# Kernel tuning notes

Measured on AMD Instinct MI355X. Metric: run time of the kernel, lower is better.

## Reference

```python
import math
import jax, jax.numpy as jnp
import numpy as np

B, C, T = 8, 512, 1024
H = 8
HD = C // H  # 64
CLIP = 4
COUT = 512


def setup_inputs() -> dict:
    key = jax.random.key(0)
    ks = jax.random.split(key, 12)
    s_qkv = math.sqrt(6.0 / (C + C))  # xavier_uniform for 1x1 conv
    queries = jax.random.normal(ks[0], (B, C, T), dtype=jnp.float32)
    Wq = jax.random.uniform(ks[1], (C, C), jnp.float32, -s_qkv, s_qkv)
    bq = jnp.zeros((C,), jnp.float32)
    Wk = jax.random.uniform(ks[2], (C, C), jnp.float32, -s_qkv, s_qkv)
    bk = jnp.zeros((C,), jnp.float32)
    Wv = jax.random.uniform(ks[3], (C, C), jnp.float32, -s_qkv, s_qkv)
    bv = jnp.zeros((C,), jnp.float32)
    Wp = jax.random.normal(ks[4], (COUT, C), jnp.float32) * (1.0 / math.sqrt(C))
    bp = jnp.zeros((COUT,), jnp.float32)
    w_std = HD ** (-0.5)
    wK = jax.random.normal(ks[5], (1, 2 * CLIP + 1, HD), jnp.float32) * w_std
    wV = jax.random.normal(ks[6], (1, 2 * CLIP + 1, HD), jnp.float32) * w_std
    return {"queries": queries, "Wq": Wq, "bq": bq, "Wk": Wk, "bk": bk,
            "Wv": Wv, "bv": bv, "Wp": Wp, "bp": bp, "wK": wK, "wV": wV}


def _get_relative_embedding(w, length):
    # w: [1, 2*CLIP+1, HD] -> [1, 2*length-1, HD]
    emb_len = 2 * length - 1
    p = max(emb_len - 2 * CLIP - 1, 0)
    pc, pf = (p + 1) // 2, p // 2  # ceil, floor of p/2
    w = jnp.pad(w, ((0, 0), (pc, pf), (0, 0)))
    idx = max(CLIP + 1 - length, 0)
    return w[:, idx:idx + emb_len]


def _rel_to_abs(x):
    # x: [B, H, L, 2L-1] -> [B, H, L, L]  (pad/shift trick)
    b, h, L, _ = x.shape
    x = jnp.pad(x, ((0, 0), (0, 0), (0, 0), (0, 1)))           # [b,h,L,2L]
    x = x.reshape(b, h, L * 2 * L)
    x = jnp.pad(x, ((0, 0), (0, 0), (0, L - 1)))
    x = x.reshape(b, h, L + 1, 2 * L - 1)
    return x[:, :, :L, L - 1:]


def _abs_to_rel(x):
    # x: [B, H, L, L] -> [B, H, L, 2L-1]
    b, h, L, _ = x.shape
    x = jnp.pad(x, ((0, 0), (0, 0), (0, 0), (0, L - 1)))       # [b,h,L,2L-1]
    x = x.reshape(b, h, L * (2 * L - 1))
    x = jnp.pad(x, ((0, 0), (0, 0), (L, 0)))
    x = x.reshape(b, h, L, 2 * L)
    return x[:, :, :, 1:]


def reference(queries, Wq, bq, Wk, bk, Wv, bv, Wp, bp, wK, wV):
    b, c, t = queries.shape
    scale = 1.0 / math.sqrt(HD)
    # 1x1-conv projections (self-attention: keys = values = queries)
    q = jnp.einsum('oc,bct->bot', Wq, queries) + bq[None, :, None]
    k = jnp.einsum('oc,bct->bot', Wk, queries) + bk[None, :, None]
    v = jnp.einsum('oc,bct->bot', Wv, queries) + bv[None, :, None]
    # [b, H, t, HD]
    q = q.reshape(b, H, HD, t).transpose(0, 1, 3, 2)
    k = k.reshape(b, H, HD, t).transpose(0, 1, 3, 2)
    v = v.reshape(b, H, HD, t).transpose(0, 1, 3, 2)
    scores = jnp.einsum('bhtd,bhsd->bhts', q, k) * scale
    # relative-position key bias
    rel_k = _get_relative_embedding(wK, t)[0]                  # [2t-1, HD]
    pos = jnp.einsum('bhtd,md->bhtm', q, rel_k)                # [b,H,t,2t-1]
    scores = scores + _rel_to_abs(pos) * scale
    alignments = jax.nn.softmax(scores, axis=-1)
    attn = jnp.einsum('bhts,bhsd->bhtd', alignments, v)
    # relative-position value bias
    rel_v = _get_relative_embedding(wV, t)[0]                  # [2t-1, HD]
    pos_rel = _abs_to_rel(alignments)                          # [b,H,t,2t-1]
    attn = attn + jnp.einsum('bhtm,md->bhtd', pos_rel, rel_v)
    attn = attn.transpose(0, 1, 3, 2).reshape(b, c, t)         # [b, C, t]
    out = jnp.einsum('oc,bct->bot', Wp, attn) + bp[None, :, None]
    return out, alignments
```

## Files before the change

### kernel.cpp

```cpp
#include <hip/hip_runtime.h>
#include <hip/hip_bf16.h>

#define BB 8
#define CC 512
#define TT 1024
#define HH 8
#define HD 64
#define CLIPW 4
#define NCOUT 512

using bf16 = __hip_bfloat16;
typedef __bf16 bf16x8_t __attribute__((ext_vector_type(8)));
typedef __bf16 bf16x4_t __attribute__((ext_vector_type(4)));
typedef float f32x4_t __attribute__((ext_vector_type(4)));

__global__ __launch_bounds__(256) void prep_w(
    const float* __restrict__ Wq, const float* __restrict__ Wk,
    const float* __restrict__ Wv, const float* __restrict__ Wp,
    bf16* __restrict__ wqf, bf16* __restrict__ wkf,
    bf16* __restrict__ wvf, bf16* __restrict__ wpf) {
  const int which = blockIdx.y;
  const float* W = (which == 0) ? Wq : (which == 1) ? Wk : (which == 2) ? Wv : Wp;
  bf16* F = (which == 0) ? wqf : (which == 1) ? wkf : (which == 2) ? wvf : wpf;
  const int gid = blockIdx.x * 256 + threadIdx.x;
  const int l = gid & 63;
  const int fid = gid >> 6;
  const int ct = fid & 15, ot = fid >> 4;
  const int sl = l & 15, g = l >> 4;
  const float* src = W + (size_t)(ot * 16 + sl) * CC + ct * 32 + g * 8;
  bf16x8_t p;
#pragma unroll
  for (int j = 0; j < 8; ++j) p[j] = (__bf16)src[j];
  *(bf16x8_t*)(F + (size_t)fid * 512 + l * 8) = p;
}

__global__ __launch_bounds__(256) void prep_x(
    const float* __restrict__ X, bf16* __restrict__ xfrag) {
  __shared__ float Xs[32][72];
  const int b = blockIdx.z, ct = blockIdx.y, tq = blockIdx.x;
  const int c0 = ct * 32, t0 = tq * 64;
  const int tid = threadIdx.x;
  {
    const int ci = tid >> 4;
    const int t4 = (tid & 15) * 4;
#pragma unroll
    for (int cp = 0; cp < 2; ++cp) {
      const int c = cp * 16 + ci;
      const float4 x4 = *(const float4*)&X[((size_t)b * CC + c0 + c) * TT + t0 + t4];
      *(float4*)&Xs[c][t4] = x4;
    }
  }
  __syncthreads();
  const int l = tid & 63, fr = tid >> 6;
  const int sl = l & 15, g = l >> 4;
  bf16x8_t p;
#pragma unroll
  for (int j = 0; j < 8; ++j) p[j] = (__bf16)Xs[g * 8 + j][fr * 16 + sl];
  *(bf16x8_t*)(xfrag + (((size_t)b * 64 + tq * 4 + fr) * 16 + ct) * 512 + l * 8) = p;
}

__global__ __launch_bounds__(256) void gemm_qkv2(
    const bf16* __restrict__ xfrag,
    const bf16* __restrict__ wqf, const bf16* __restrict__ wkf,
    const bf16* __restrict__ wvf,
    const float* __restrict__ bq, const float* __restrict__ bk,
    const float* __restrict__ bv,
    bf16* __restrict__ qfrag, bf16* __restrict__ kfrag, bf16* __restrict__ vfrag) {
  __shared__ __align__(16) float Cs[64 * 68];
  const int y  = blockIdx.y;
  const int m  = y >> 3;
  const int o0 = (y & 7) * 64;
  const int t0 = blockIdx.x * 64;
  const int b  = blockIdx.z;
  const bf16* WF = (m == 0) ? wqf : (m == 1) ? wkf : wvf;
  const float* bias = (m == 0) ? bq : (m == 1) ? bk : bv;

  const int tid = threadIdx.x;
  const int w = tid >> 6, l = tid & 63, g = l >> 4, sl = l & 15;
  const int wr = w >> 1, wc = w & 1;
  const int ot0 = (o0 >> 4) + wr * 2;
  const int tt0 = (t0 >> 4) + wc * 2;

  f32x4_t acc[2][2] = {};
#pragma unroll 4
  for (int ct = 0; ct < 16; ++ct) {
    bf16x8_t a[2], bb[2];
#pragma unroll
    for (int mm = 0; mm < 2; ++mm)
      a[mm] = *(const bf16x8_t*)(WF + ((size_t)(ot0 + mm) * 16 + ct) * 512 + l * 8);
#pragma unroll
    for (int nn = 0; nn < 2; ++nn)
      bb[nn] = *(const bf16x8_t*)(xfrag + (((size_t)b * 64 + tt0 + nn) * 16 + ct) * 512 + l * 8);
#pragma unroll
    for (int mm = 0; mm < 2; ++mm)
#pragma unroll
      for (int nn = 0; nn < 2; ++nn)
        acc[mm][nn] = __builtin_amdgcn_mfma_f32_16x16x32_bf16(a[mm], bb[nn], acc[mm][nn], 0, 0, 0);
  }

#pragma unroll
  for (int mm = 0; mm < 2; ++mm)
#pragma unroll
    for (int nn = 0; nn < 2; ++nn)
#pragma unroll
      for (int r = 0; r < 4; ++r)
        Cs[(wr * 32 + mm * 16 + 4 * g + r) * 68 + wc * 32 + nn * 16 + sl] = acc[mm][nn][r];
  __syncthreads();

  const int hh2 = o0 >> 6;
  const int bh  = b * HH + hh2;
  const int fr = tid >> 6, l2 = tid & 63;
  const int sl2 = l2 & 15, g2 = l2 >> 4;
  if (m == 0) {
#pragma unroll
    for (int kh = 0; kh < 2; ++kh) {
      bf16x8_t p;
#pragma unroll
      for (int j = 0; j < 8; ++j) {
        const int d = kh * 32 + g2 * 8 + j;
        p[j] = (__bf16)(Cs[d * 68 + fr * 16 + sl2] + bias[o0 + d]);
      }
      *(bf16x8_t*)(qfrag + (((size_t)bh * 64 + (t0 >> 4) + fr) * 2 + kh) * 512 + l2 * 8) = p;
    }
  } else if (m == 1) {
    bf16* dpf = kfrag + (((size_t)bh * 64 + (t0 >> 4) + fr) * 2) * 512;
#pragma unroll
    for (int half = 0; half < 2; ++half) {
      bf16x8_t p;
#pragma unroll
      for (int j = 0; j < 8; ++j) {
        const int d = half * 32 + g2 * 8 + j;
        p[j] = (__bf16)(Cs[d * 68 + fr * 16 + sl2] + bias[o0 + d]);
      }
      *(bf16x8_t*)(dpf + half * 512 + l2 * 8) = p;
    }
  } else {
    const int dt = fr;
    const int d  = dt * 16 + sl2;
    const float bv_ = bias[o0 + d];
#pragma unroll
    for (int i2p = 0; i2p < 2; ++i2p) {
      const int i2 = (t0 >> 5) + i2p;
      bf16x8_t p;
#pragma unroll
      for (int j = 0; j < 8; ++j) {
        const int tloc = i2p * 32 + g2 * 8 + j;
        p[j] = (__bf16)(Cs[d * 68 + tloc] + bv_);
      }
      *(bf16x8_t*)(vfrag + ((((size_t)bh * 32 + i2) * 4 + dt) * 64 + l2) * 8) = p;
    }
  }
}

__global__ __launch_bounds__(256) void gemm_out2(
    const bf16* __restrict__ attnfrag, const bf16* __restrict__ wpf,
    const float* __restrict__ bp, float* __restrict__ out) {
  __shared__ __align__(16) float Cs[64 * 68];
  const int o0 = blockIdx.y * 64;
  const int t0 = blockIdx.x * 64;
  const int b  = blockIdx.z;
  const int tid = threadIdx.x;
  const int w = tid >> 6, l = tid & 63, g = l >> 4, sl = l & 15;
  const int wr = w >> 1, wc = w & 1;
  const int ot0 = (o0 >> 4) + wr * 2;
  const int tt0 = (t0 >> 4) + wc * 2;

  f32x4_t acc[2][2] = {};
#pragma unroll 4
  for (int ct = 0; ct < 16; ++ct) {
    bf16x8_t a[2], bb[2];
#pragma unroll
    for (int mm = 0; mm < 2; ++mm)
      a[mm] = *(const bf16x8_t*)(wpf + ((size_t)(ot0 + mm) * 16 + ct) * 512 + l * 8);
#pragma unroll
    for (int nn = 0; nn < 2; ++nn)
      bb[nn] = *(const bf16x8_t*)(attnfrag + (((size_t)b * 64 + tt0 + nn) * 16 + ct) * 512 + l * 8);
#pragma unroll
    for (int mm = 0; mm < 2; ++mm)
#pragma unroll
      for (int nn = 0; nn < 2; ++nn)
        acc[mm][nn] = __builtin_amdgcn_mfma_f32_16x16x32_bf16(a[mm], bb[nn], acc[mm][nn], 0, 0, 0);
  }

#pragma unroll
  for (int mm = 0; mm < 2; ++mm)
#pragma unroll
    for (int nn = 0; nn < 2; ++nn)
#pragma unroll
      for (int r = 0; r < 4; ++r)
        Cs[(wr * 32 + mm * 16 + 4 * g + r) * 68 + wc * 32 + nn * 16 + sl] = acc[mm][nn][r];
  __syncthreads();

  const int o = tid >> 2, tq = tid & 3;
  const float bv_ = bp[o0 + o];
  float* dp = out + ((size_t)b * NCOUT + o0 + o) * TT + t0 + tq * 16;
#pragma unroll
  for (int i4 = 0; i4 < 4; ++i4) {
    f32x4_t v = *(const f32x4_t*)&Cs[o * 68 + tq * 16 + i4 * 4];
    v[0] += bv_; v[1] += bv_; v[2] += bv_; v[3] += bv_;
    *(f32x4_t*)(dp + i4 * 4) = v;
  }
}

__global__ __launch_bounds__(256, 4) void attn_v12(
    const bf16* __restrict__ qfrag, const bf16* __restrict__ kfrag,
    const bf16* __restrict__ vfrag,
    const float* __restrict__ wK, const float* __restrict__ wV,
    float* __restrict__ align_out, bf16* __restrict__ attnfrag) {
  const int fi   = blockIdx.x;
  const int xcd  = fi & 7;
  const int k2   = fi >> 3;
  const int bh   = ((k2 >> 6) << 3) + xcd;
  const int qblk = k2 & 63;
  const int b = bh >> 3, h = bh & 7;
  const int q0 = qblk * 16;

  const int tid = threadIdx.x;
  const int w = tid >> 6, l = tid & 63, g = l >> 4, ql = l & 15;
  const int qabs  = q0 + ql;
  const int sbase = w * 256;

  __shared__ __align__(16) char smem[39424];
  __bf16* eL    = (__bf16*)smem;
  float* bandv  = (float*)(smem + 33792);
  float* bandP  = (float*)(smem + 36864);
  float* redbuf = (float*)(smem + 39168);
  float* invL   = (float*)(smem + 33792);
  float* obuf   = (float*)smem;
  float* stg    = (float*)(smem + 17408);

  for (int i = tid; i < 576; i += 256) bandP[i] = 0.f;

  const bf16* qfb = qfrag + (((size_t)bh * 64 + (q0 >> 4)) * 2) * 512 + l * 8;
  const bf16x8_t qa0 = *(const bf16x8_t*)qfb;
  const bf16x8_t qa1 = *(const bf16x8_t*)(qfb + 512);

  {
    const int j = (ql < 9) ? ql : 0;
    const float* wkr = wK + j * HD + g * 8;
    const f32x4_t w0 = *(const f32x4_t*)wkr;
    const f32x4_t w1 = *(const f32x4_t*)(wkr + 4);
    const f32x4_t w2 = *(const f32x4_t*)(wkr + 32);
    const f32x4_t w3 = *(const f32x4_t*)(wkr + 36);
    bf16x8_t ka0, ka1;
#pragma unroll
    for (int i = 0; i < 4; ++i) {
      ka0[i] = (__bf16)w0[i]; ka0[4 + i] = (__bf16)w1[i];
      ka1[i] = (__bf16)w2[i]; ka1[4 + i] = (__bf16)w3[i];
    }
    f32x4_t bacc = {0.f, 0.f, 0.f, 0.f};
    bacc = __builtin_amdgcn_mfma_f32_16x16x32_bf16(ka0, qa0, bacc, 0, 0, 0);
    bacc = __builtin_amdgcn_mfma_f32_16x16x32_bf16(ka1, qa1, bacc, 0, 0, 0);
#pragma unroll
    for (int r = 0; r < 4; ++r)
      if (4 * g + r < 9) bandv[(w * 16 + ql) * 12 + 4 * g + r] = bacc[r];
  }

  float ls = 0.f;
  bf16x4_t stash[16];
  const int erow = (w * 16 + ql) * 264;
  const bf16* kfb = kfrag + (((size_t)bh * 64 + w * 16) * 2) * 512 + l * 8;
#pragma unroll
  for (int st = 0; st < 16; ++st) {
    const bf16x8_t k0 = *(const bf16x8_t*)(kfb + (size_t)st * 1024);
    const bf16x8_t k1 = *(const bf16x8_t*)(kfb + (size_t)st * 1024 + 512);
    f32x4_t a = {0.f, 0.f, 0.f, 0.f};
    a = __builtin_amdgcn_mfma_f32_16x16x32_bf16(k0, qa0, a, 0, 0, 0);
    a = __builtin_amdgcn_mfma_f32_16x16x32_bf16(k1, qa1, a, 0, 0, 0);
    const int s0t = sbase + st * 16;
    const bool near = (s0t + 15 >= q0 - CLIPW) && (s0t <= q0 + 15 + CLIPW);
#pragma unroll
    for (int r = 0; r < 4; ++r) {
      float x = a[r];
      if (near) {
        const int delta = s0t + 4 * g + r - qabs;
        if ((unsigned)(delta + CLIPW) <= 2 * CLIPW)
          x += bandv[(w * 16 + ql) * 12 + delta + CLIPW];
      }
      const float e = __expf(x * 0.125f);
      stash[st][r] = (__bf16)e;
      ls += e;
    }
    *(bf16x4_t*)&eL[erow + st * 16 + 4 * g] = stash[st];
  }
  ls += __shfl_xor(ls, 16);
  ls += __shfl_xor(ls, 32);
  if (l < 16) redbuf[w * 16 + ql] = ls;
  __syncthreads();
  const float inv = 1.0f / (redbuf[ql] + redbuf[16 + ql] + redbuf[32 + ql] + redbuf[48 + ql]);
  if (l < 16) invL[w * 16 + l] = inv;

#pragma unroll
  for (int st = 0; st < 16; ++st) {
    const int s0t = sbase + st * 16;
    const bool near = (s0t + 15 >= q0 - CLIPW) && (s0t <= q0 + 15 + CLIPW);
    if (near) {
#pragma unroll
      for (int r = 0; r < 4; ++r) {
        const int delta = s0t + 4 * g + r - qabs;
        if ((unsigned)(delta + CLIPW) <= 2 * CLIPW)
          bandP[ql * 36 + delta + CLIPW] = (float)stash[st][r] * inv;
      }
    }
  }

  f32x4_t oacc[4] = {};
  const bf16* vfb = vfrag + (((size_t)bh * 32 + w * 8) * 4) * 512 + l * 8;
  float* abase = align_out + ((size_t)bh * TT + q0) * TT + sbase + l * 4;
#pragma unroll
  for (int i2 = 0; i2 < 8; ++i2) {
    const bf16x8_t pb = *(const bf16x8_t*)&eL[erow + i2 * 32 + 8 * g];
#pragma unroll
    for (int dt = 0; dt < 4; ++dt) {
      const bf16x8_t va = *(const bf16x8_t*)(vfb + ((size_t)i2 * 4 + dt) * 512);
      oacc[dt] = __builtin_amdgcn_mfma_f32_16x16x32_bf16(va, pb, oacc[dt], 0, 0, 0);
    }
#pragma unroll
    for (int qq = 0; qq < 2; ++qq) {
      const int q = i2 * 2 + qq;
      const float iq = invL[w * 16 + q];
      const bf16x4_t e4 = *(const bf16x4_t*)&eL[(w * 16 + q) * 264 + l * 4];
      f32x4_t p4;
      p4[0] = (float)e4[0] * iq;
      p4[1] = (float)e4[1] * iq;
      p4[2] = (float)e4[2] * iq;
      p4[3] = (float)e4[3] * iq;
      __builtin_nontemporal_store(p4, (f32x4_t*)(abase + (size_t)q * TT));
    }
  }
#pragma unroll
  for (int dt = 0; dt < 4; ++dt) {
    oacc[dt][0] *= inv; oacc[dt][1] *= inv;
    oacc[dt][2] *= inv; oacc[dt][3] *= inv;
  }

  __syncthreads();

#pragma unroll
  for (int dt = 0; dt < 4; ++dt)
    *(f32x4_t*)&obuf[w * 1088 + ql * 68 + dt * 16 + 4 * g] = oacc[dt];
  __syncthreads();

  if (w == 0) {
    f32x4_t osum[4];
#pragma unroll
    for (int dt = 0; dt < 4; ++dt) {
      const int off = ql * 68 + dt * 16 + 4 * g;
      osum[dt] = *(const f32x4_t*)&obuf[off] + *(const f32x4_t*)&obuf[1088 + off] +
                 *(const f32x4_t*)&obuf[2176 + off] + *(const f32x4_t*)&obuf[3264 + off];
    }
    const f32x4_t b0 = *(const f32x4_t*)&bandP[ql * 36 + g * 8];
    const f32x4_t b1 = *(const f32x4_t*)&bandP[ql * 36 + g * 8 + 4];
    bf16x8_t pbb;
#pragma unroll
    for (int i = 0; i < 4; ++i) {
      pbb[i] = (__bf16)b0[i];
      pbb[4 + i] = (__bf16)b1[i];
    }
#pragma unroll
    for (int dt = 0; dt < 4; ++dt) {
      bf16x8_t wa;
#pragma unroll
      for (int jj = 0; jj < 8; ++jj) {
        const int j = g * 8 + jj;
        wa[jj] = (__bf16)((j < 9) ? wV[j * HD + dt * 16 + ql] : 0.f);
      }
      osum[dt] = __builtin_amdgcn_mfma_f32_16x16x32_bf16(wa, pbb, osum[dt], 0, 0, 0);
    }
#pragma unroll
    for (int dt = 0; dt < 4; ++dt)
#pragma unroll
      for (int r = 0; r < 4; ++r)
        stg[(dt * 16 + 4 * g + r) * 17 + ql] = osum[dt][r];
#pragma unroll
    for (int ctl = 0; ctl < 2; ++ctl) {
      bf16x8_t p;
#pragma unroll
      for (int j = 0; j < 8; ++j)
        p[j] = (__bf16)stg[(ctl * 32 + g * 8 + j) * 17 + ql];
      *(bf16x8_t*)(attnfrag +
                   (((size_t)b * 64 + (q0 >> 4)) * 16 + h * 2 + ctl) * 512 + l * 8) = p;
    }
  }
}

extern "C" void kernel_launch(void* const* d_in, const int* in_sizes, int n_in,
                              void* d_out, int out_size, void* d_ws, size_t ws_size,
                              hipStream_t stream) {
  const float* X  = (const float*)d_in[0];
  const float* Wq = (const float*)d_in[1];
  const float* bq = (const float*)d_in[2];
  const float* Wk = (const float*)d_in[3];
  const float* bk = (const float*)d_in[4];
  const float* Wv = (const float*)d_in[5];
  const float* bv = (const float*)d_in[6];
  const float* Wp = (const float*)d_in[7];
  const float* bp = (const float*)d_in[8];
  const float* wK = (const float*)d_in[9];
  const float* wV = (const float*)d_in[10];

  float* out       = (float*)d_out;
  float* align_out = out + (size_t)BB * NCOUT * TT;

  const size_t SZ = (size_t)BB * HH * TT * HD;
  const size_t WF = 512 * 512;
  bf16* qfrag    = (bf16*)d_ws;
  bf16* kfrag    = qfrag + SZ;
  bf16* vfrag    = qfrag + 2 * SZ;
  bf16* attnfrag = qfrag + 3 * SZ;
  bf16* xfrag    = qfrag + 4 * SZ;
  bf16* wqf      = qfrag + 5 * SZ;
  bf16* wkf      = wqf + WF;
  bf16* wvf      = wkf + WF;
  bf16* wpf      = wvf + WF;

  prep_w<<<dim3(128, 4), 256, 0, stream>>>(Wq, Wk, Wv, Wp, wqf, wkf, wvf, wpf);
  prep_x<<<dim3(16, 16, BB), 256, 0, stream>>>(X, xfrag);
  gemm_qkv2<<<dim3(16, 24, BB), 256, 0, stream>>>(
      xfrag, wqf, wkf, wvf, bq, bk, bv, qfrag, kfrag, vfrag);
  attn_v12<<<dim3(4096), 256, 0, stream>>>(
      qfrag, kfrag, vfrag, wK, wV, align_out, attnfrag);
  gemm_out2<<<dim3(16, 8, BB), 256, 0, stream>>>(attnfrag, wpf, bp, out);
}
```

Before: 144.3 us.

## Remap GEMM grids for XCD batch locality and raise MFMA wave priority

Flattens the prep_x, QKV GEMM and output GEMM grids to 1D and derives the batch index from the low three bits of the block id. Under round-robin dispatch across the eight XCDs, each batch then stays on one XCD, keeping its activations in that die's L2. The attention kernel also wraps its MFMA sequences in s_setprio(1)/s_setprio(0) so waves issuing matrix ops get scheduling priority over waves doing memory and exp work. The remap assumes blocks are dispatched to XCDs round-robin, and the priority hints may do nothing or disturb latency hiding.

Measured after the change: 147.9 us. 1.02x slower.

```diff
diff --git a/kernel.cpp b/kernel.cpp
--- a/kernel.cpp
+++ b/kernel.cpp
@@ -37,7 +37,10 @@
 __global__ __launch_bounds__(256) void prep_x(
     const float* __restrict__ X, bf16* __restrict__ xfrag) {
   __shared__ float Xs[32][72];
-  const int b = blockIdx.z, ct = blockIdx.y, tq = blockIdx.x;
+  const int fi = blockIdx.x;
+  const int b = fi & 7;
+  const int k = fi >> 3;
+  const int ct = k & 15, tq = k >> 4;
   const int c0 = ct * 32, t0 = tq * 64;
   const int tid = threadIdx.x;
   {
@@ -67,11 +70,14 @@
     const float* __restrict__ bv,
     bf16* __restrict__ qfrag, bf16* __restrict__ kfrag, bf16* __restrict__ vfrag) {
   __shared__ __align__(16) float Cs[64 * 68];
-  const int y  = blockIdx.y;
+  const int fi = blockIdx.x;
+  const int b  = fi & 7;
+  const int k2 = fi >> 3;
+  const int y  = k2 % 24;
+  const int xb = k2 / 24;
   const int m  = y >> 3;
   const int o0 = (y & 7) * 64;
-  const int t0 = blockIdx.x * 64;
-  const int b  = blockIdx.z;
+  const int t0 = xb * 64;
   const bf16* WF = (m == 0) ? wqf : (m == 1) ? wkf : wvf;
   const float* bias = (m == 0) ? bq : (m == 1) ? bk : bv;
 
@@ -156,9 +162,11 @@
     const bf16* __restrict__ attnfrag, const bf16* __restrict__ wpf,
     const float* __restrict__ bp, float* __restrict__ out) {
   __shared__ __align__(16) float Cs[64 * 68];
-  const int o0 = blockIdx.y * 64;
-  const int t0 = blockIdx.x * 64;
-  const int b  = blockIdx.z;
+  const int fi = blockIdx.x;
+  const int b  = fi & 7;
+  const int k2 = fi >> 3;
+  const int o0 = (k2 & 7) * 64;
+  const int t0 = (k2 >> 3) * 64;
   const int tid = threadIdx.x;
   const int w = tid >> 6, l = tid & 63, g = l >> 4, sl = l & 15;
   const int wr = w >> 1, wc = w & 1;
@@ -202,7 +210,7 @@
   }
 }
 
-__global__ __launch_bounds__(256, 4) void attn_v12(
+__global__ __launch_bounds__(256, 4) void attn_v13(
     const bf16* __restrict__ qfrag, const bf16* __restrict__ kfrag,
     const bf16* __restrict__ vfrag,
     const float* __restrict__ wK, const float* __restrict__ wV,
@@ -265,8 +273,10 @@
     const bf16x8_t k0 = *(const bf16x8_t*)(kfb + (size_t)st * 1024);
     const bf16x8_t k1 = *(const bf16x8_t*)(kfb + (size_t)st * 1024 + 512);
     f32x4_t a = {0.f, 0.f, 0.f, 0.f};
+    __builtin_amdgcn_s_setprio(1);
     a = __builtin_amdgcn_mfma_f32_16x16x32_bf16(k0, qa0, a, 0, 0, 0);
     a = __builtin_amdgcn_mfma_f32_16x16x32_bf16(k1, qa1, a, 0, 0, 0);
+    __builtin_amdgcn_s_setprio(0);
     const int s0t = sbase + st * 16;
     const bool near = (s0t + 15 >= q0 - CLIPW) && (s0t <= q0 + 15 + CLIPW);
 #pragma unroll
@@ -310,11 +320,13 @@
 #pragma unroll
   for (int i2 = 0; i2 < 8; ++i2) {
     const bf16x8_t pb = *(const bf16x8_t*)&eL[erow + i2 * 32 + 8 * g];
+    __builtin_amdgcn_s_setprio(1);
 #pragma unroll
     for (int dt = 0; dt < 4; ++dt) {
       const bf16x8_t va = *(const bf16x8_t*)(vfb + ((size_t)i2 * 4 + dt) * 512);
       oacc[dt] = __builtin_amdgcn_mfma_f32_16x16x32_bf16(va, pb, oacc[dt], 0, 0, 0);
     }
+    __builtin_amdgcn_s_setprio(0);
 #pragma unroll
     for (int qq = 0; qq < 2; ++qq) {
       const int q = i2 * 2 + qq;
@@ -415,10 +427,10 @@
   bf16* wpf      = wvf + WF;
 
   prep_w<<<dim3(128, 4), 256, 0, stream>>>(Wq, Wk, Wv, Wp, wqf, wkf, wvf, wpf);
-  prep_x<<<dim3(16, 16, BB), 256, 0, stream>>>(X, xfrag);
-  gemm_qkv2<<<dim3(16, 24, BB), 256, 0, stream>>>(
+  prep_x<<<dim3(2048), 256, 0, stream>>>(X, xfrag);
+  gemm_qkv2<<<dim3(3072), 256, 0, stream>>>(
       xfrag, wqf, wkf, wvf, bq, bk, bv, qfrag, kfrag, vfrag);
-  attn_v12<<<dim3(4096), 256, 0, stream>>>(
+  attn_v13<<<dim3(4096), 256, 0, stream>>>(
       qfrag, kfrag, vfrag, wK, wV, align_out, attnfrag);
-  gemm_out2<<<dim3(16, 8, BB), 256, 0, stream>>>(attnfrag, wpf, bp, out);
-}
+  gemm_out2<<<dim3(1024), 256, 0, stream>>>(attnfrag, wpf, bp, out);
+}
```

## Halve attention LDS footprint by staging probabilities in two rounds, raise occupancy

Applied to the files above, without the earlier changes.

The attention kernel now writes the bf16 exp tile to shared memory in two halves of 128 columns each, processing PV MFMA and alignment stores per half, cutting LDS from ~39KB to ~23KB. The launch bound is raised from 4 to 6 blocks per CU to exploit the smaller footprint, and the staging buffer for the final output is stored as bf16. The alignment store pattern changes so each half-wave writes 128 contiguous floats per row. The tighter register budget may cause spills given the 16-entry stash array.

Result: slower. 170.1 us (+17.8%).

```diff
diff --git a/kernel.cpp b/kernel.cpp
--- a/kernel.cpp
+++ b/kernel.cpp
@@ -202,7 +202,7 @@
   }
 }
 
-__global__ __launch_bounds__(256, 4) void attn_v12(
+__global__ __launch_bounds__(256, 6) void attn_v14(
     const bf16* __restrict__ qfrag, const bf16* __restrict__ kfrag,
     const bf16* __restrict__ vfrag,
     const float* __restrict__ wK, const float* __restrict__ wV,
@@ -220,14 +220,14 @@
   const int qabs  = q0 + ql;
   const int sbase = w * 256;
 
-  __shared__ __align__(16) char smem[39424];
-  __bf16* eL    = (__bf16*)smem;
-  float* bandv  = (float*)(smem + 33792);
-  float* bandP  = (float*)(smem + 36864);
-  float* redbuf = (float*)(smem + 39168);
-  float* invL   = (float*)(smem + 33792);
+  __shared__ __align__(16) char smem[23040];
+  __bf16* eLh   = (__bf16*)smem;
   float* obuf   = (float*)smem;
-  float* stg    = (float*)(smem + 17408);
+  float* bandP  = (float*)(smem + 17408);
+  float* redbuf = (float*)(smem + 19712);
+  float* bandv  = (float*)(smem + 19968);
+  float* invL   = (float*)(smem + 19968);
+  __bf16* stg   = (__bf16*)(smem + 19968);
 
   for (int i = tid; i < 576; i += 256) bandP[i] = 0.f;
 
@@ -258,7 +258,6 @@
 
   float ls = 0.f;
   bf16x4_t stash[16];
-  const int erow = (w * 16 + ql) * 264;
   const bf16* kfb = kfrag + (((size_t)bh * 64 + w * 16) * 2) * 512 + l * 8;
 #pragma unroll
   for (int st = 0; st < 16; ++st) {
@@ -281,7 +280,6 @@
       stash[st][r] = (__bf16)e;
       ls += e;
     }
-    *(bf16x4_t*)&eL[erow + st * 16 + 4 * g] = stash[st];
   }
   ls += __shfl_xor(ls, 16);
   ls += __shfl_xor(ls, 32);
@@ -306,26 +304,37 @@
 
   f32x4_t oacc[4] = {};
   const bf16* vfb = vfrag + (((size_t)bh * 32 + w * 8) * 4) * 512 + l * 8;
-  float* abase = align_out + ((size_t)bh * TT + q0) * TT + sbase + l * 4;
-#pragma unroll
-  for (int i2 = 0; i2 < 8; ++i2) {
-    const bf16x8_t pb = *(const bf16x8_t*)&eL[erow + i2 * 32 + 8 * g];
-#pragma unroll
-    for (int dt = 0; dt < 4; ++dt) {
-      const bf16x8_t va = *(const bf16x8_t*)(vfb + ((size_t)i2 * 4 + dt) * 512);
-      oacc[dt] = __builtin_amdgcn_mfma_f32_16x16x32_bf16(va, pb, oacc[dt], 0, 0, 0);
-    }
-#pragma unroll
-    for (int qq = 0; qq < 2; ++qq) {
-      const int q = i2 * 2 + qq;
-      const float iq = invL[w * 16 + q];
-      const bf16x4_t e4 = *(const bf16x4_t*)&eL[(w * 16 + q) * 264 + l * 4];
-      f32x4_t p4;
-      p4[0] = (float)e4[0] * iq;
-      p4[1] = (float)e4[1] * iq;
-      p4[2] = (float)e4[2] * iq;
-      p4[3] = (float)e4[3] * iq;
-      __builtin_nontemporal_store(p4, (f32x4_t*)(abase + (size_t)q * TT));
+  const int erow = (w * 16 + ql) * 132;
+  const int qhalf = l >> 5;
+  const int c32 = (l & 31) * 4;
+  float* abase = align_out + ((size_t)bh * TT + q0) * TT + sbase;
+#pragma unroll
+  for (int rd = 0; rd < 2; ++rd) {
+#pragma unroll
+    for (int stl = 0; stl < 8; ++stl)
+      *(bf16x4_t*)&eLh[erow + stl * 16 + 4 * g] = stash[rd * 8 + stl];
+#pragma unroll
+    for (int i2l = 0; i2l < 4; ++i2l) {
+      const bf16x8_t pb = *(const bf16x8_t*)&eLh[erow + i2l * 32 + 8 * g];
+#pragma unroll
+      for (int dt = 0; dt < 4; ++dt) {
+        const bf16x8_t va =
+            *(const bf16x8_t*)(vfb + ((size_t)(rd * 4 + i2l) * 4 + dt) * 512);
+        oacc[dt] = __builtin_amdgcn_mfma_f32_16x16x32_bf16(va, pb, oacc[dt], 0, 0, 0);
+      }
+#pragma unroll
+      for (int k = 0; k < 2; ++k) {
+        const int it = i2l * 2 + k;
+        const int q = it * 2 + qhalf;
+        const float iq = invL[w * 16 + q];
+        const bf16x4_t e4 = *(const bf16x4_t*)&eLh[(w * 16 + q) * 132 + c32];
+        f32x4_t p4;
+        p4[0] = (float)e4[0] * iq;
+        p4[1] = (float)e4[1] * iq;
+        p4[2] = (float)e4[2] * iq;
+        p4[3] = (float)e4[3] * iq;
+        __builtin_nontemporal_store(p4, (f32x4_t*)(abase + (size_t)q * TT + rd * 128 + c32));
+      }
     }
   }
 #pragma unroll
@@ -371,13 +380,13 @@
     for (int dt = 0; dt < 4; ++dt)
 #pragma unroll
       for (int r = 0; r < 4; ++r)
-        stg[(dt * 16 + 4 * g + r) * 17 + ql] = osum[dt][r];
+        stg[(dt * 16 + 4 * g + r) * 17 + ql] = (__bf16)osum[dt][r];
 #pragma unroll
     for (int ctl = 0; ctl < 2; ++ctl) {
       bf16x8_t p;
 #pragma unroll
       for (int j = 0; j < 8; ++j)
-        p[j] = (__bf16)stg[(ctl * 32 + g * 8 + j) * 17 + ql];
+        p[j] = stg[(ctl * 32 + g * 8 + j) * 17 + ql];
       *(bf16x8_t*)(attnfrag +
                    (((size_t)b * 64 + (q0 >> 4)) * 16 + h * 2 + ctl) * 512 + l * 8) = p;
     }
@@ -418,7 +427,7 @@
   prep_x<<<dim3(16, 16, BB), 256, 0, stream>>>(X, xfrag);
   gemm_qkv2<<<dim3(16, 24, BB), 256, 0, stream>>>(
       xfrag, wqf, wkf, wvf, bq, bk, bv, qfrag, kfrag, vfrag);
-  attn_v12<<<dim3(4096), 256, 0, stream>>>(
+  attn_v14<<<dim3(4096), 256, 0, stream>>>(
       qfrag, kfrag, vfrag, wK, wV, align_out, attnfrag);
   gemm_out2<<<dim3(16, 8, BB), 256, 0, stream>>>(attnfrag, wpf, bp, out);
 }
```
